# Kernel tuning notes

Measured on AMD Instinct MI355X. Metric: run time of the kernel, lower is better.

## Reference

```python
import jax, jax.numpy as jnp
import numpy as np

B, N, D, E, H, K = 2, 2048, 1024, 8, 2048, 2


def setup_inputs() -> dict:
    key = jax.random.key(0)
    ks = jax.random.split(key, 5)
    s = 0.02  # init scale
    return {
        "x": jax.random.normal(ks[0], (B, N, D), dtype=jnp.float32),
        "w_gate": jax.random.normal(ks[1], (D, E), dtype=jnp.float32) * s,
        "b_gate": jnp.zeros((E,), dtype=jnp.float32),
        "w1": jax.random.normal(ks[2], (E, D, H), dtype=jnp.float32) * s,
        "b1": jnp.zeros((E, H), dtype=jnp.float32),
        "w2": jax.random.normal(ks[3], (E, H, D), dtype=jnp.float32) * s,
        "b2": jnp.zeros((E, D), dtype=jnp.float32),
    }


def reference(x, w_gate, b_gate, w1, b1, w2, b2):
    b, n, d = x.shape
    T = b * n
    xf = x.reshape(T, d)                                   # (T, D)
    # --- top-k routing ---
    logits = xf @ w_gate + b_gate                          # (T, E)
    topk_logits, topk_idx = jax.lax.top_k(logits, K)       # (T, K)
    topk_gates = jax.nn.softmax(topk_logits, axis=-1)      # softmax over selected experts
    entropy = -(topk_gates * jnp.log(jnp.clip(topk_gates, 1e-8, None))).sum(-1).mean()
    # scatter top-k gates into full (T, E) gate matrix (zeros for unselected)
    gates = jnp.zeros_like(logits).at[jnp.arange(T)[:, None], topk_idx].add(topk_gates)
    # --- expert MLPs (dense over experts; gates zero out unselected) ---
    h = jax.nn.relu(jnp.einsum('td,edh->eth', xf, w1) + b1[:, None, :])  # (E, T, H)
    y = jnp.einsum('eth,ehd->etd', h, w2) + b2[:, None, :]               # (E, T, D)
    out = jnp.einsum('etd,te->td', y, gates).reshape(b, n, d)
    return out, entropy
```

## Files before the change

### kernel.cpp

```cpp
#include <hip/hip_runtime.h>

#define T_TOK 4096
#define D_DIM 1024
#define E_EXP 8
#define H_DIM 2048
#define CAP   9216
#define TILES_M 72

typedef __attribute__((ext_vector_type(8))) short bf16x8;
typedef __attribute__((ext_vector_type(4))) float f32x4;

__device__ inline unsigned short f2bf(float f) {
    unsigned int u = __float_as_uint(f);
    unsigned int r = (u + 0x7fffu + ((u >> 16) & 1u)) >> 16;
    return (unsigned short)r;
}

#define GLD_LDS16(g, l)                                                        \
    __builtin_amdgcn_global_load_lds(                                          \
        (const __attribute__((address_space(1))) void*)(g),                    \
        (__attribute__((address_space(3))) void*)(l), 16, 0, 0)

__global__ __launch_bounds__(256) void tcvt_kernel(const float* __restrict__ src,
                                                   unsigned short* __restrict__ dst,
                                                   int R, int C) {
    __shared__ float tile[64][65];
    size_t eo = (size_t)blockIdx.z * R * C;
    src += eo; dst += eo;
    int tx = threadIdx.x & 15, ty = threadIdx.x >> 4;
    int c0 = blockIdx.x * 64, r0 = blockIdx.y * 64;
    #pragma unroll
    for (int i = 0; i < 4; i++) {
        int row = ty + i * 16;
        float4 v = *(const float4*)&src[(size_t)(r0 + row) * C + c0 + tx * 4];
        tile[row][tx * 4 + 0] = v.x;
        tile[row][tx * 4 + 1] = v.y;
        tile[row][tx * 4 + 2] = v.z;
        tile[row][tx * 4 + 3] = v.w;
    }
    __syncthreads();
    #pragma unroll
    for (int i = 0; i < 4; i++) {
        int cc = ty + i * 16;
        int rr = tx * 4;
        ushort4 o;
        o.x = f2bf(tile[rr + 0][cc]);
        o.y = f2bf(tile[rr + 1][cc]);
        o.z = f2bf(tile[rr + 2][cc]);
        o.w = f2bf(tile[rr + 3][cc]);
        *(ushort4*)&dst[(size_t)(c0 + cc) * R + r0 + rr] = o;
    }
}

__global__ __launch_bounds__(256) void gating_kernel(
    const float* __restrict__ xf, const float* __restrict__ wg,
    const float* __restrict__ bg, unsigned short* __restrict__ xb,
    int* __restrict__ tk_e, float* __restrict__ tk_g,
    float* __restrict__ ent_part)
{
    __shared__ float ents[4];
    int wave = threadIdx.x >> 6, lane = threadIdx.x & 63;
    int t = blockIdx.x * 4 + wave;
    const float* xr = xf + (size_t)t * D_DIM;
    unsigned short* xbr = xb + (size_t)t * D_DIM;
    float acc[8] = {0.f,0.f,0.f,0.f,0.f,0.f,0.f,0.f};
    for (int i = 0; i < 16; i++) {
        int d = lane + i * 64;
        float xv = xr[d];
        xbr[d] = f2bf(xv);
        const float4* wr = (const float4*)(wg + (size_t)d * 8);
        float4 w0 = wr[0], w1 = wr[1];
        acc[0] += xv * w0.x; acc[1] += xv * w0.y; acc[2] += xv * w0.z; acc[3] += xv * w0.w;
        acc[4] += xv * w1.x; acc[5] += xv * w1.y; acc[6] += xv * w1.z; acc[7] += xv * w1.w;
    }
    #pragma unroll
    for (int s = 1; s < 64; s <<= 1) {
        #pragma unroll
        for (int e = 0; e < 8; e++) acc[e] += __shfl_xor(acc[e], s, 64);
    }
    if (lane == 0) {
        float l[8];
        #pragma unroll
        for (int e = 0; e < 8; e++) l[e] = acc[e] + bg[e];
        int i0 = 0;
        #pragma unroll
        for (int e = 1; e < 8; e++) if (l[e] > l[i0]) i0 = e;
        int i1 = (i0 == 0) ? 1 : 0;
        #pragma unroll
        for (int e = 0; e < 8; e++) if (e != i0 && l[e] > l[i1]) i1 = e;
        float z  = expf(l[i1] - l[i0]);
        float p0 = 1.0f / (1.0f + z);
        float p1 = z / (1.0f + z);
        float ent = -(p0 * logf(fmaxf(p0, 1e-8f)) + p1 * logf(fmaxf(p1, 1e-8f)));
        ents[wave] = ent;
        tk_e[t * 2 + 0] = i0; tk_g[t * 2 + 0] = p0;
        tk_e[t * 2 + 1] = i1; tk_g[t * 2 + 1] = p1;
    }
    __syncthreads();
    if (threadIdx.x == 0)
        ent_part[blockIdx.x] = ents[0] + ents[1] + ents[2] + ents[3];
}

__global__ __launch_bounds__(1024) void route_kernel(
    const int* __restrict__ tk_e, const float* __restrict__ tk_g,
    int* __restrict__ off, int* __restrict__ slot_token,
    float* __restrict__ slot_gate, int* __restrict__ slot_of,
    const float* __restrict__ ent_part, float* __restrict__ ent_out)
{
    __shared__ int wt[16][8];
    __shared__ int wx[16][8];
    __shared__ int base[9];
    __shared__ int tot[8];
    __shared__ float es[16];

    int tid = threadIdx.x, wid = tid >> 6, lane = tid & 63;
    int i0 = tid * 8;
    int ev[8];
    *(int4*)&ev[0] = *(const int4*)&tk_e[i0];
    *(int4*)&ev[4] = *(const int4*)&tk_e[i0 + 4];

    float s = ent_part[tid];
    #pragma unroll
    for (int d = 1; d < 64; d <<= 1) s += __shfl_xor(s, d, 64);
    if (lane == 0) es[wid] = s;

    unsigned own[4] = {0u, 0u, 0u, 0u};
    #pragma unroll
    for (int j = 0; j < 8; j++) {
        int e = ev[j];
        int reg = ((e < 4) ? 0 : 2) + (e & 1);
        own[reg] += 1u << (((e >> 1) & 1) * 16);
    }
    unsigned inc[4] = {own[0], own[1], own[2], own[3]};
    #pragma unroll
    for (int d = 1; d < 64; d <<= 1) {
        #pragma unroll
        for (int k = 0; k < 4; k++) {
            unsigned t = __shfl_up(inc[k], d, 64);
            if (lane >= d) inc[k] += t;
        }
    }
    if (lane == 63) {
        #pragma unroll
        for (int e = 0; e < 8; e++) {
            int reg = ((e < 4) ? 0 : 2) + (e & 1);
            wt[wid][e] = (inc[reg] >> (((e >> 1) & 1) * 16)) & 0xFFFF;
        }
    }
    __syncthreads();
    if (tid == 0) {
        int o = 0;
        for (int e = 0; e < 8; e++) {
            int run = 0;
            for (int w = 0; w < 16; w++) { wx[w][e] = run; run += wt[w][e]; }
            tot[e] = run;
            base[e] = o;
            off[e] = o;
            o += (run + 127) & ~127;
        }
        base[8] = o;
        off[8] = o;
        float se = 0.f;
        for (int w = 0; w < 16; w++) se += es[w];
        *ent_out = se * (1.0f / T_TOK);
    }
    __syncthreads();

    #pragma unroll
    for (int e = 0; e < 8; e++) {
        int p0 = base[e] + tot[e], p1 = base[e + 1];
        for (int i = p0 + tid; i < p1; i += 1024) slot_token[i] = -1;
    }

    unsigned run[4] = {0u, 0u, 0u, 0u};
    #pragma unroll
    for (int j = 0; j < 8; j++) {
        int e = ev[j];
        int reg = ((e < 4) ? 0 : 2) + (e & 1);
        int sh = ((e >> 1) & 1) * 16;
        int lx = (int)(((inc[reg] - own[reg]) >> sh) & 0xFFFF);
        int lr = (int)((run[reg] >> sh) & 0xFFFF);
        int slot = base[e] + wx[wid][e] + lx + lr;
        run[reg] += 1u << sh;
        int i = i0 + j;
        slot_token[slot] = i >> 1;
        slot_gate[slot] = tk_g[i];
        slot_of[i] = slot;
    }
}

template<int KD, int ND, bool GATHER, bool RELU>
__global__ __launch_bounds__(256) void gemm_kernel(
    const unsigned short* __restrict__ Ag, const unsigned short* __restrict__ Bw,
    const float* __restrict__ bias, const int* __restrict__ off,
    const int* __restrict__ slot_token, unsigned short* __restrict__ Out)
{
    constexpr int NT = KD / 32;
    __shared__ __align__(16) unsigned short As[2][128 * 32];
    __shared__ __align__(16) unsigned short Bs[2][128 * 32];

    int s0 = blockIdx.x * 128;
    if (s0 >= off[E_EXP]) return;
    int e = 0;
    while (s0 >= off[e + 1]) e++;
    int n0 = blockIdx.y * 128;

    int tid = threadIdx.x;
    int wave = tid >> 6, lane = tid & 63;
    int lrow = lane & 15, quad = lane >> 4;
    int srow = lane >> 2;
    int scol = ((lane & 3) ^ ((srow >> 1) & 3)) * 8;

    int r0 = 16 * wave + srow, r1 = r0 + 64;
    const unsigned short* a0;
    const unsigned short* a1;
    if constexpr (GATHER) {
        int t0 = slot_token[s0 + r0]; if (t0 < 0) t0 = 0;
        int t1 = slot_token[s0 + r1]; if (t1 < 0) t1 = 0;
        a0 = Ag + (size_t)t0 * KD + scol;
        a1 = Ag + (size_t)t1 * KD + scol;
    } else {
        a0 = Ag + (size_t)(s0 + r0) * KD + scol;
        a1 = Ag + (size_t)(s0 + r1) * KD + scol;
    }
    const unsigned short* wb = Bw + (size_t)e * ND * KD;
    const unsigned short* bp0 = wb + (size_t)(n0 + r0) * KD + scol;
    const unsigned short* bp1 = wb + (size_t)(n0 + r1) * KD + scol;

    int stA0 = (16 * wave) * 32;
    int stA1 = (64 + 16 * wave) * 32;

    f32x4 acc[4][4];
    #pragma unroll
    for (int mi = 0; mi < 4; mi++)
        #pragma unroll
        for (int ni = 0; ni < 4; ni++) acc[mi][ni] = (f32x4){0.f, 0.f, 0.f, 0.f};

    int wr = (wave >> 1) * 64, wc = (wave & 1) * 64;
    int g = (quad ^ ((lrow >> 1) & 3)) * 8;

    auto STAGE = [&](int b, int k) {
        GLD_LDS16(a0 + k,  &As[b][stA0]);
        GLD_LDS16(a1 + k,  &As[b][stA1]);
        GLD_LDS16(bp0 + k, &Bs[b][stA0]);
        GLD_LDS16(bp1 + k, &Bs[b][stA1]);
    };
    auto COMPUTE = [&](int b) {
        bf16x8 af[4], bfr[4];
        #pragma unroll
        for (int i = 0; i < 4; i++) {
            af[i]  = *(const bf16x8*)&As[b][(wr + i * 16 + lrow) * 32 + g];
            bfr[i] = *(const bf16x8*)&Bs[b][(wc + i * 16 + lrow) * 32 + g];
        }
        __builtin_amdgcn_s_setprio(1);
        #pragma unroll
        for (int mi = 0; mi < 4; mi++)
            #pragma unroll
            for (int ni = 0; ni < 4; ni++)
                acc[mi][ni] = __builtin_amdgcn_mfma_f32_16x16x32_bf16(
                    af[mi], bfr[ni], acc[mi][ni], 0, 0, 0);
        __builtin_amdgcn_s_setprio(0);
    };

    STAGE(0, 0);
    STAGE(1, 32);
    for (int t = 0; t < NT - 1; ++t) {
        asm volatile("s_waitcnt vmcnt(4)" ::: "memory");
        asm volatile("s_barrier" ::: "memory");
        COMPUTE(t & 1);
        asm volatile("s_barrier" ::: "memory");
        if (t + 2 < NT) STAGE(t & 1, (t + 2) * 32);
    }
    asm volatile("s_waitcnt vmcnt(0)" ::: "memory");
    asm volatile("s_barrier" ::: "memory");
    COMPUTE((NT - 1) & 1);
    asm volatile("s_barrier" ::: "memory");

    float bv[4];
    #pragma unroll
    for (int ni = 0; ni < 4; ni++)
        bv[ni] = bias[(size_t)e * ND + n0 + wc + ni * 16 + lrow];
    unsigned short* w = &As[0][0] + wave * 1024;
    #pragma unroll
    for (int mi = 0; mi < 4; mi++) {
        #pragma unroll
        for (int ni = 0; ni < 4; ni++)
            #pragma unroll
            for (int rr = 0; rr < 4; rr++) {
                float v = acc[mi][ni][rr] + bv[ni];
                if constexpr (RELU) v = fmaxf(v, 0.0f);
                w[(quad * 4 + rr) * 64 + ni * 16 + lrow] = f2bf(v);
            }
        int rd = lane >> 3, cc = (lane & 7) * 8;
        bf16x8 v0 = *(const bf16x8*)&w[rd * 64 + cc];
        bf16x8 v1 = *(const bf16x8*)&w[(8 + rd) * 64 + cc];
        size_t rowg = (size_t)(s0 + wr + mi * 16 + rd) * ND + n0 + wc + cc;
        *(bf16x8*)&Out[rowg] = v0;
        *(bf16x8*)&Out[rowg + 8 * (size_t)ND] = v1;
    }
}

__global__ __launch_bounds__(256) void combine_kernel(
    const unsigned short* __restrict__ Yb, const int* __restrict__ slot_of,
    const float* __restrict__ tk_g, float* __restrict__ out)
{
    int t = blockIdx.x * 2 + (threadIdx.x >> 7);
    int j = threadIdx.x & 127;
    int sA = slot_of[t * 2], sB = slot_of[t * 2 + 1];
    float gA = tk_g[t * 2], gB = tk_g[t * 2 + 1];
    uint4 va = *(const uint4*)(Yb + (size_t)sA * D_DIM + j * 8);
    uint4 vb = *(const uint4*)(Yb + (size_t)sB * D_DIM + j * 8);
    const unsigned int* pa = (const unsigned int*)&va;
    const unsigned int* pb = (const unsigned int*)&vb;
    float o[8];
    #pragma unroll
    for (int i = 0; i < 4; i++) {
        float a_lo = __uint_as_float(pa[i] << 16);
        float a_hi = __uint_as_float(pa[i] & 0xffff0000u);
        float b_lo = __uint_as_float(pb[i] << 16);
        float b_hi = __uint_as_float(pb[i] & 0xffff0000u);
        o[i * 2 + 0] = gA * a_lo + gB * b_lo;
        o[i * 2 + 1] = gA * a_hi + gB * b_hi;
    }
    float* op = out + (size_t)t * D_DIM + j * 8;
    ((float4*)op)[0] = make_float4(o[0], o[1], o[2], o[3]);
    ((float4*)op)[1] = make_float4(o[4], o[5], o[6], o[7]);
}

extern "C" void kernel_launch(void* const* d_in, const int* in_sizes, int n_in,
                              void* d_out, int out_size, void* d_ws, size_t ws_size,
                              hipStream_t stream)
{
    const float* xf = (const float*)d_in[0];
    const float* wg = (const float*)d_in[1];
    const float* bg = (const float*)d_in[2];
    const float* w1 = (const float*)d_in[3];
    const float* b1 = (const float*)d_in[4];
    const float* w2 = (const float*)d_in[5];
    const float* b2 = (const float*)d_in[6];
    float* out = (float*)d_out;

    char* p = (char*)d_ws;
    int* off    = (int*)p;
    int* tk_e   = off + 16;
    float* tk_g = (float*)(tk_e + T_TOK * 2);
    int* slot_token = (int*)(tk_g + T_TOK * 2);
    float* slot_gate = (float*)(slot_token + CAP);
    int* slot_of = (int*)(slot_gate + CAP);
    float* ent_part = (float*)(slot_of + T_TOK * 2);
    size_t ofs = ((size_t)((char*)(ent_part + T_TOK / 4) - p) + 255) & ~(size_t)255;
    unsigned short* xb  = (unsigned short*)(p + ofs); ofs += (size_t)T_TOK * D_DIM * 2;
    unsigned short* w1t = (unsigned short*)(p + ofs); ofs += (size_t)E_EXP * D_DIM * H_DIM * 2;
    unsigned short* w2t = (unsigned short*)(p + ofs); ofs += (size_t)E_EXP * H_DIM * D_DIM * 2;
    unsigned short* Hb  = (unsigned short*)(p + ofs); ofs += (size_t)CAP * H_DIM * 2;
    unsigned short* Yb  = w1t;

    gating_kernel<<<T_TOK / 4, 256, 0, stream>>>(xf, wg, bg, xb, tk_e, tk_g, ent_part);
    route_kernel<<<1, 1024, 0, stream>>>(tk_e, tk_g, off, slot_token, slot_gate, slot_of,
                                         ent_part, out + (size_t)T_TOK * D_DIM);
    tcvt_kernel<<<dim3(H_DIM / 64, D_DIM / 64, E_EXP), 256, 0, stream>>>(w1, w1t, D_DIM, H_DIM);
    tcvt_kernel<<<dim3(D_DIM / 64, H_DIM / 64, E_EXP), 256, 0, stream>>>(w2, w2t, H_DIM, D_DIM);
    gemm_kernel<D_DIM, H_DIM, true, true>
        <<<dim3(TILES_M, H_DIM / 128), 256, 0, stream>>>(xb, w1t, b1, off, slot_token, Hb);
    gemm_kernel<H_DIM, D_DIM, false, false>
        <<<dim3(TILES_M, D_DIM / 128), 256, 0, stream>>>(Hb, w2t, b2, off, slot_token, Yb);
    combine_kernel<<<T_TOK / 2, 256, 0, stream>>>(Yb, slot_of, tk_g, out);
}
```

Before: 331.4 us.

## Widen expert GEMM tile to 128x256 with per-wave 64x128 accumulators

The grouped expert GEMMs now use a 128x256 output tile instead of 128x128. Each wave holds 4x8 MFMA accumulators and computes them in two halves that reuse the A fragments. This halves the number of times A rows are re-staged and improves arithmetic intensity per LDS load. In exchange it doubles accumulator registers, adds B staging traffic per block, and halves the grid: the first GEMM drops to 72x8 blocks and the second to 72x4, which lowers the number of blocks available to fill the CUs.

```diff
diff --git a/kernel.cpp b/kernel.cpp
--- a/kernel.cpp
+++ b/kernel.cpp
@@ -190,20 +190,20 @@
 }
 
 template<int KD, int ND, bool GATHER, bool RELU>
-__global__ __launch_bounds__(256) void gemm_kernel(
+__global__ __launch_bounds__(256, 2) void gemm_kernel(
     const unsigned short* __restrict__ Ag, const unsigned short* __restrict__ Bw,
     const float* __restrict__ bias, const int* __restrict__ off,
     const int* __restrict__ slot_token, unsigned short* __restrict__ Out)
 {
     constexpr int NT = KD / 32;
     __shared__ __align__(16) unsigned short As[2][128 * 32];
-    __shared__ __align__(16) unsigned short Bs[2][128 * 32];
+    __shared__ __align__(16) unsigned short Bs[2][256 * 32];
 
     int s0 = blockIdx.x * 128;
     if (s0 >= off[E_EXP]) return;
     int e = 0;
     while (s0 >= off[e + 1]) e++;
-    int n0 = blockIdx.y * 128;
+    int n0 = blockIdx.y * 256;
 
     int tid = threadIdx.x;
     int wave = tid >> 6, lane = tid & 63;
@@ -225,18 +225,20 @@
     }
     const unsigned short* wb = Bw + (size_t)e * ND * KD;
     const unsigned short* bp0 = wb + (size_t)(n0 + r0) * KD + scol;
-    const unsigned short* bp1 = wb + (size_t)(n0 + r1) * KD + scol;
+    const unsigned short* bp1 = wb + (size_t)(n0 + 64 + r0) * KD + scol;
+    const unsigned short* bp2 = wb + (size_t)(n0 + 128 + r0) * KD + scol;
+    const unsigned short* bp3 = wb + (size_t)(n0 + 192 + r0) * KD + scol;
 
     int stA0 = (16 * wave) * 32;
     int stA1 = (64 + 16 * wave) * 32;
 
-    f32x4 acc[4][4];
+    f32x4 acc[4][8];
     #pragma unroll
     for (int mi = 0; mi < 4; mi++)
         #pragma unroll
-        for (int ni = 0; ni < 4; ni++) acc[mi][ni] = (f32x4){0.f, 0.f, 0.f, 0.f};
-
-    int wr = (wave >> 1) * 64, wc = (wave & 1) * 64;
+        for (int ni = 0; ni < 8; ni++) acc[mi][ni] = (f32x4){0.f, 0.f, 0.f, 0.f};
+
+    int wr = (wave >> 1) * 64, wc = (wave & 1) * 128;
     int g = (quad ^ ((lrow >> 1) & 3)) * 8;
 
     auto STAGE = [&](int b, int k) {
@@ -244,14 +246,17 @@
         GLD_LDS16(a1 + k,  &As[b][stA1]);
         GLD_LDS16(bp0 + k, &Bs[b][stA0]);
         GLD_LDS16(bp1 + k, &Bs[b][stA1]);
+        GLD_LDS16(bp2 + k, &Bs[b][(128 + 16 * wave) * 32]);
+        GLD_LDS16(bp3 + k, &Bs[b][(192 + 16 * wave) * 32]);
     };
     auto COMPUTE = [&](int b) {
         bf16x8 af[4], bfr[4];
         #pragma unroll
-        for (int i = 0; i < 4; i++) {
-            af[i]  = *(const bf16x8*)&As[b][(wr + i * 16 + lrow) * 32 + g];
+        for (int i = 0; i < 4; i++)
+            af[i] = *(const bf16x8*)&As[b][(wr + i * 16 + lrow) * 32 + g];
+        #pragma unroll
+        for (int i = 0; i < 4; i++)
             bfr[i] = *(const bf16x8*)&Bs[b][(wc + i * 16 + lrow) * 32 + g];
-        }
         __builtin_amdgcn_s_setprio(1);
         #pragma unroll
         for (int mi = 0; mi < 4; mi++)
@@ -260,12 +265,23 @@
                 acc[mi][ni] = __builtin_amdgcn_mfma_f32_16x16x32_bf16(
                     af[mi], bfr[ni], acc[mi][ni], 0, 0, 0);
         __builtin_amdgcn_s_setprio(0);
+        #pragma unroll
+        for (int i = 0; i < 4; i++)
+            bfr[i] = *(const bf16x8*)&Bs[b][(wc + 64 + i * 16 + lrow) * 32 + g];
+        __builtin_amdgcn_s_setprio(1);
+        #pragma unroll
+        for (int mi = 0; mi < 4; mi++)
+            #pragma unroll
+            for (int ni = 0; ni < 4; ni++)
+                acc[mi][4 + ni] = __builtin_amdgcn_mfma_f32_16x16x32_bf16(
+                    af[mi], bfr[ni], acc[mi][4 + ni], 0, 0, 0);
+        __builtin_amdgcn_s_setprio(0);
     };
 
     STAGE(0, 0);
     STAGE(1, 32);
     for (int t = 0; t < NT - 1; ++t) {
-        asm volatile("s_waitcnt vmcnt(4)" ::: "memory");
+        asm volatile("s_waitcnt vmcnt(6)" ::: "memory");
         asm volatile("s_barrier" ::: "memory");
         COMPUTE(t & 1);
         asm volatile("s_barrier" ::: "memory");
@@ -276,27 +292,31 @@
     COMPUTE((NT - 1) & 1);
     asm volatile("s_barrier" ::: "memory");
 
-    float bv[4];
-    #pragma unroll
-    for (int ni = 0; ni < 4; ni++)
+    float bv[8];
+    #pragma unroll
+    for (int ni = 0; ni < 8; ni++)
         bv[ni] = bias[(size_t)e * ND + n0 + wc + ni * 16 + lrow];
-    unsigned short* w = &As[0][0] + wave * 1024;
+    unsigned short* w = &As[0][0] + wave * 2048;
     #pragma unroll
     for (int mi = 0; mi < 4; mi++) {
         #pragma unroll
-        for (int ni = 0; ni < 4; ni++)
+        for (int ni = 0; ni < 8; ni++)
             #pragma unroll
             for (int rr = 0; rr < 4; rr++) {
                 float v = acc[mi][ni][rr] + bv[ni];
                 if constexpr (RELU) v = fmaxf(v, 0.0f);
-                w[(quad * 4 + rr) * 64 + ni * 16 + lrow] = f2bf(v);
+                w[(quad * 4 + rr) * 128 + ni * 16 + lrow] = f2bf(v);
             }
         int rd = lane >> 3, cc = (lane & 7) * 8;
-        bf16x8 v0 = *(const bf16x8*)&w[rd * 64 + cc];
-        bf16x8 v1 = *(const bf16x8*)&w[(8 + rd) * 64 + cc];
+        bf16x8 v0a = *(const bf16x8*)&w[rd * 128 + cc];
+        bf16x8 v0b = *(const bf16x8*)&w[rd * 128 + 64 + cc];
+        bf16x8 v1a = *(const bf16x8*)&w[(8 + rd) * 128 + cc];
+        bf16x8 v1b = *(const bf16x8*)&w[(8 + rd) * 128 + 64 + cc];
         size_t rowg = (size_t)(s0 + wr + mi * 16 + rd) * ND + n0 + wc + cc;
-        *(bf16x8*)&Out[rowg] = v0;
-        *(bf16x8*)&Out[rowg + 8 * (size_t)ND] = v1;
+        *(bf16x8*)&Out[rowg] = v0a;
+        *(bf16x8*)&Out[rowg + 64] = v0b;
+        *(bf16x8*)&Out[rowg + 8 * (size_t)ND] = v1a;
+        *(bf16x8*)&Out[rowg + 8 * (size_t)ND + 64] = v1b;
     }
 }
 
@@ -361,8 +381,8 @@
     tcvt_kernel<<<dim3(H_DIM / 64, D_DIM / 64, E_EXP), 256, 0, stream>>>(w1, w1t, D_DIM, H_DIM);
     tcvt_kernel<<<dim3(D_DIM / 64, H_DIM / 64, E_EXP), 256, 0, stream>>>(w2, w2t, H_DIM, D_DIM);
     gemm_kernel<D_DIM, H_DIM, true, true>
-        <<<dim3(TILES_M, H_DIM / 128), 256, 0, stream>>>(xb, w1t, b1, off, slot_token, Hb);
+        <<<dim3(TILES_M, H_DIM / 256), 256, 0, stream>>>(xb, w1t, b1, off, slot_token, Hb);
     gemm_kernel<H_DIM, D_DIM, false, false>
-        <<<dim3(TILES_M, D_DIM / 128), 256, 0, stream>>>(Hb, w2t, b2, off, slot_token, Yb);
+        <<<dim3(TILES_M, D_DIM / 256), 256, 0, stream>>>(Hb, w2t, b2, off, slot_token, Yb);
     combine_kernel<<<T_TOK / 2, 256, 0, stream>>>(Yb, slot_of, tk_g, out);
 }
```

New measurement: 343.1 us. 3.5% more time.
